# Optimization experiments

Hardware: AMD Instinct MI355X
Metric: run time of the kernel (lower is better)

Reference implementation:

```python
import jax, jax.numpy as jnp
import numpy as np

NODE_DIM = 128
N_NODES = 100000
N_EDGES = 600000


def setup_inputs() -> dict:
    key = jax.random.key(0)
    k_x, k_e, k_w1, k_b1, k_w2, k_b2 = jax.random.split(key, 6)
    x = jax.random.normal(k_x, (N_NODES, NODE_DIM), dtype=jnp.float32)
    edge_index = jax.random.randint(k_e, (2, N_EDGES), 0, N_NODES, dtype=jnp.int64)
    # nn.Linear default init: U(-1/sqrt(fan_in), 1/sqrt(fan_in))
    lim1 = 1.0 / np.sqrt(2 * NODE_DIM)
    W1 = jax.random.uniform(k_w1, (2 * NODE_DIM, NODE_DIM), minval=-lim1, maxval=lim1, dtype=jnp.float32)
    b1 = jax.random.uniform(k_b1, (NODE_DIM,), minval=-lim1, maxval=lim1, dtype=jnp.float32)
    lim2 = 1.0 / np.sqrt(NODE_DIM)
    W2 = jax.random.uniform(k_w2, (NODE_DIM, 1), minval=-lim2, maxval=lim2, dtype=jnp.float32)
    b2 = jax.random.uniform(k_b2, (1,), minval=-lim2, maxval=lim2, dtype=jnp.float32)
    return {"x": x, "edge_index": edge_index, "W1": W1, "b1": b1, "W2": W2, "b2": b2}


def reference(x, edge_index, W1, b1, W2, b2):
    src = edge_index[0]
    dst = edge_index[1]
    # [E, 2*node_dim] gathered pair features
    pair = jnp.concatenate([x[src], x[dst]], axis=-1)
    h = jax.nn.relu(pair @ W1 + b1)          # [E, node_dim]
    s = jax.nn.sigmoid(h @ W2 + b2)          # [E, 1]
    return s.squeeze(-1)                      # [E]
```

## Files before the change

### kernel.cpp

```cpp
#include <hip/hip_runtime.h>
#include <hip/hip_bf16.h>
#include <stdint.h>

#define NODE_DIM 128
#define N_NODES  100000
#define N_EDGES  600000
#define NOUT     256

typedef __bf16 bf16x8 __attribute__((ext_vector_type(8)));
typedef float  f32x4  __attribute__((ext_vector_type(4)));

static __device__ inline unsigned pack2_bf16(float a, float b) {
    unsigned short ua = __builtin_bit_cast(unsigned short, (__bf16)a);
    unsigned short ub = __builtin_bit_cast(unsigned short, (__bf16)b);
    return (unsigned)ua | ((unsigned)ub << 16);
}

static __device__ __forceinline__ void async_copy16(const float* g, void* l) {
    __builtin_amdgcn_global_load_lds(
        (__attribute__((address_space(1))) void*)(uintptr_t)g,
        (__attribute__((address_space(3))) void*)(uint32_t)(uintptr_t)l,
        16, 0, 0);
}

__global__ void wprep_kernel(const float* __restrict__ W1, __bf16* __restrict__ Wt) {
    int i = blockIdx.x * 256 + threadIdx.x;
    if (i >= NOUT * NODE_DIM) return;
    int kp = i >> 7;
    int n  = i & 127;
    float v = W1[i];
    int np = (kp < NODE_DIM) ? n  : (n + NODE_DIM);
    int k  = (kp < NODE_DIM) ? kp : (kp - NODE_DIM);
    Wt[np * NODE_DIM + k] = (__bf16)v;
}

#define MT   64
#define ELD  264

__global__ __launch_bounds__(256)
void gemm_pre_kernel(const float* __restrict__ x, const __bf16* __restrict__ Wt,
                     const float* __restrict__ b1, __bf16* __restrict__ AB) {
    __shared__ __align__(16) char lds_raw[MT * ELD * 2];
    float* Xf = (float*)lds_raw;
    __bf16 (*Ls)[ELD] = (__bf16 (*)[ELD])lds_raw;

    const int t    = threadIdx.x;
    const int wave = t >> 6;
    const int lane = t & 63;
    const int lm   = lane & 15;
    const int q    = lane >> 4;
    const int m0   = blockIdx.x * MT;
    const int n0   = wave * 64;

#pragma unroll
    for (int i = 0; i < 8; ++i) {
        const int sbase = i * 256 + wave * 64;
        const int s  = sbase + lane;
        const int R  = s >> 5;
        const int p  = s & 31;
        const int cg = p ^ (R & 7);
        int gr = m0 + R;
        if (gr > N_NODES - 1) gr = N_NODES - 1;
        async_copy16(x + (size_t)gr * NODE_DIM + cg * 4, &Xf[(size_t)sbase * 4]);
    }

    bf16x8 bfr[4][4];
#pragma unroll
    for (int nt = 0; nt < 4; ++nt) {
        const int n = n0 + nt * 16 + lm;
#pragma unroll
        for (int ks = 0; ks < 4; ++ks)
            bfr[nt][ks] = __builtin_bit_cast(bf16x8,
                *(const uint4*)(Wt + (size_t)n * NODE_DIM + ks * 32 + q * 8));
    }

    __syncthreads();

    f32x4 acc[4][4];
#pragma unroll
    for (int i = 0; i < 4; ++i)
#pragma unroll
        for (int j = 0; j < 4; ++j)
            acc[i][j] = (f32x4){0.f, 0.f, 0.f, 0.f};

#pragma unroll
    for (int mt = 0; mt < 4; ++mt) {
        const int R  = mt * 16 + lm;
        const int rs = R & 7;
#pragma unroll
        for (int ks = 0; ks < 4; ++ks) {
            const int c0 = ks * 8 + q * 2;
            const float4 f0 = *(const float4*)&Xf[(R * 32 + (c0 ^ rs)) * 4];
            const float4 f1 = *(const float4*)&Xf[(R * 32 + ((c0 + 1) ^ rs)) * 4];
            uint4 p;
            p.x = pack2_bf16(f0.x, f0.y);
            p.y = pack2_bf16(f0.z, f0.w);
            p.z = pack2_bf16(f1.x, f1.y);
            p.w = pack2_bf16(f1.z, f1.w);
            bf16x8 af = __builtin_bit_cast(bf16x8, p);
#pragma unroll
            for (int nt = 0; nt < 4; ++nt)
                acc[mt][nt] = __builtin_amdgcn_mfma_f32_16x16x32_bf16(
                    af, bfr[nt][ks], acc[mt][nt], 0, 0, 0);
        }
    }

    __syncthreads();

#pragma unroll
    for (int nt = 0; nt < 4; ++nt) {
        const int n = n0 + nt * 16 + lm;
        const float bias = (n < NODE_DIM) ? b1[n] : 0.f;
#pragma unroll
        for (int mt = 0; mt < 4; ++mt) {
#pragma unroll
            for (int r = 0; r < 4; ++r)
                Ls[mt * 16 + q * 4 + r][n] = (__bf16)(acc[mt][nt][r] + bias);
        }
    }
    __syncthreads();

    const int c8 = (t & 31) * 8;
#pragma unroll
    for (int i = 0; i < 8; ++i) {
        const int row = i * 8 + (t >> 5);
        const int m = m0 + row;
        if (m < N_NODES)
            *(uint4*)(AB + (size_t)m * NOUT + c8) = *(const uint4*)(&Ls[row][c8]);
    }
}

__global__ __launch_bounds__(256)
void edge_score_kernel(const __bf16* __restrict__ AB, const int* __restrict__ idx,
                       const float* __restrict__ W2, const float* __restrict__ b2,
                       float* __restrict__ out) {
    const int t      = threadIdx.x;
    const int sub    = t & 15;
    const int g0     = (blockIdx.x * 256 + t) >> 4;
    const int stride = (gridDim.x * 256) >> 4;

    float w[8];
#pragma unroll
    for (int j = 0; j < 8; ++j) w[j] = W2[sub * 8 + j];
    const float bias2 = b2[0];

    for (int e = g0; e < N_EDGES; e += 2 * stride) {
        const int e1   = e + stride;
        const bool h1  = e1 < N_EDGES;
        const int s0 = idx[e];
        const int d0 = idx[N_EDGES + e];
        const int s1 = h1 ? idx[e1] : s0;
        const int d1 = h1 ? idx[N_EDGES + e1] : d0;

        const uint4 av0 = *(const uint4*)(AB + (size_t)s0 * NOUT + sub * 8);
        const uint4 bv0 = *(const uint4*)(AB + (size_t)d0 * NOUT + NODE_DIM + sub * 8);
        const uint4 av1 = *(const uint4*)(AB + (size_t)s1 * NOUT + sub * 8);
        const uint4 bv1 = *(const uint4*)(AB + (size_t)d1 * NOUT + NODE_DIM + sub * 8);

        const unsigned* au0 = (const unsigned*)&av0;
        const unsigned* bu0 = (const unsigned*)&bv0;
        const unsigned* au1 = (const unsigned*)&av1;
        const unsigned* bu1 = (const unsigned*)&bv1;
        float p0 = 0.f, p1 = 0.f;
#pragma unroll
        for (int j = 0; j < 4; ++j) {
            float a0 = __builtin_bit_cast(float, au0[j] << 16);
            float a1 = __builtin_bit_cast(float, au0[j] & 0xffff0000u);
            float c0 = __builtin_bit_cast(float, bu0[j] << 16);
            float c1 = __builtin_bit_cast(float, bu0[j] & 0xffff0000u);
            p0 = fmaf(fmaxf(a0 + c0, 0.f), w[2 * j],     p0);
            p0 = fmaf(fmaxf(a1 + c1, 0.f), w[2 * j + 1], p0);
            float e0 = __builtin_bit_cast(float, au1[j] << 16);
            float e1f= __builtin_bit_cast(float, au1[j] & 0xffff0000u);
            float f0 = __builtin_bit_cast(float, bu1[j] << 16);
            float f1 = __builtin_bit_cast(float, bu1[j] & 0xffff0000u);
            p1 = fmaf(fmaxf(e0 + f0, 0.f), w[2 * j],     p1);
            p1 = fmaf(fmaxf(e1f+ f1, 0.f), w[2 * j + 1], p1);
        }
        p0 += __shfl_xor(p0, 1);  p1 += __shfl_xor(p1, 1);
        p0 += __shfl_xor(p0, 2);  p1 += __shfl_xor(p1, 2);
        p0 += __shfl_xor(p0, 4);  p1 += __shfl_xor(p1, 4);
        p0 += __shfl_xor(p0, 8);  p1 += __shfl_xor(p1, 8);
        if (sub == 0) {
            out[e] = 1.f / (1.f + __expf(-(p0 + bias2)));
            if (h1) out[e1] = 1.f / (1.f + __expf(-(p1 + bias2)));
        }
    }
}

__global__ __launch_bounds__(128)
void naive_edge_kernel(const float* __restrict__ x, const int* __restrict__ idx,
                       const float* __restrict__ W1, const float* __restrict__ b1,
                       const float* __restrict__ W2, const float* __restrict__ b2,
                       float* __restrict__ out) {
    __shared__ float pair[2 * NODE_DIM];
    __shared__ float red[2];
    int e = blockIdx.x;
    int t = threadIdx.x;
    int s = idx[e], d = idx[N_EDGES + e];
    pair[t]            = x[(size_t)s * NODE_DIM + t];
    pair[NODE_DIM + t] = x[(size_t)d * NODE_DIM + t];
    __syncthreads();
    float acc = b1[t];
    for (int k = 0; k < 2 * NODE_DIM; ++k)
        acc = fmaf(pair[k], W1[k * NODE_DIM + t], acc);
    float c = fmaxf(acc, 0.f) * W2[t];
#pragma unroll
    for (int m = 1; m < 64; m <<= 1) c += __shfl_xor(c, m);
    if ((t & 63) == 0) red[t >> 6] = c;
    __syncthreads();
    if (t == 0) out[e] = 1.f / (1.f + __expf(-(red[0] + red[1] + b2[0])));
}

extern "C" void kernel_launch(void* const* d_in, const int* in_sizes, int n_in,
                              void* d_out, int out_size, void* d_ws, size_t ws_size,
                              hipStream_t stream) {
    const float* x   = (const float*)d_in[0];
    const int*   idx = (const int*)d_in[1];
    const float* W1  = (const float*)d_in[2];
    const float* b1  = (const float*)d_in[3];
    const float* W2  = (const float*)d_in[4];
    const float* b2  = (const float*)d_in[5];
    float* out = (float*)d_out;

    const size_t ab_bytes = (size_t)N_NODES * NOUT * sizeof(__bf16);
    const size_t wt_bytes = (size_t)NOUT * NODE_DIM * sizeof(__bf16);

    if (ws_size >= ab_bytes + wt_bytes) {
        __bf16* AB = (__bf16*)d_ws;
        __bf16* Wt = (__bf16*)((char*)d_ws + ab_bytes);
        hipLaunchKernelGGL(wprep_kernel, dim3(128), dim3(256), 0, stream, W1, Wt);
        hipLaunchKernelGGL(gemm_pre_kernel, dim3((N_NODES + MT - 1) / MT), dim3(256),
                           0, stream, x, Wt, b1, AB);
        hipLaunchKernelGGL(edge_score_kernel, dim3(2048), dim3(256), 0, stream,
                           AB, idx, W2, b2, out);
    } else {
        hipLaunchKernelGGL(naive_edge_kernel, dim3(N_EDGES), dim3(128), 0, stream,
                           x, idx, W1, b1, W2, b2, out);
    }
}
```

Baseline: 154.5 us.

## Quantize per-node projection tables to int8 with per-row scales

The precompute kernel now quantizes each node's projected src and dst halves to unsigned 8-bit values with a per-row absmax scale, instead of storing bf16. The edge kernel gathers 8-byte int8 chunks plus the scalar scales and dequantizes them with FMAs. This halves the gathered bytes per edge and the table footprint, aiming to cut memory and cache traffic. It adds quantization error, which could affect accuracy tolerance, plus some extra per-element integer unpacking work.

```diff
diff --git a/kernel.cpp b/kernel.cpp
--- a/kernel.cpp
+++ b/kernel.cpp
@@ -39,7 +39,9 @@
 
 __global__ __launch_bounds__(256)
 void gemm_pre_kernel(const float* __restrict__ x, const __bf16* __restrict__ Wt,
-                     const float* __restrict__ b1, __bf16* __restrict__ AB) {
+                     const float* __restrict__ b1,
+                     unsigned char* __restrict__ Ai, unsigned char* __restrict__ Bi,
+                     float* __restrict__ sA, float* __restrict__ sB) {
     __shared__ __align__(16) char lds_raw[MT * ELD * 2];
     float* Xf = (float*)lds_raw;
     __bf16 (*Ls)[ELD] = (__bf16 (*)[ELD])lds_raw;
@@ -120,18 +122,50 @@
     }
     __syncthreads();
 
-    const int c8 = (t & 31) * 8;
-#pragma unroll
-    for (int i = 0; i < 8; ++i) {
-        const int row = i * 8 + (t >> 5);
+    const int grp = t >> 4;
+    const int sub = t & 15;
+#pragma unroll
+    for (int pass = 0; pass < 8; ++pass) {
+        const int hr   = pass * 16 + grp;
+        const int row  = hr >> 1;
+        const int half = hr & 1;
+        const uint4 v = *(const uint4*)(&Ls[row][half * 128 + sub * 8]);
+        const unsigned* vu = (const unsigned*)&v;
+        float f[8];
+#pragma unroll
+        for (int i = 0; i < 4; ++i) {
+            f[2 * i]     = __builtin_bit_cast(float, vu[i] << 16);
+            f[2 * i + 1] = __builtin_bit_cast(float, vu[i] & 0xffff0000u);
+        }
+        float am = 0.f;
+#pragma unroll
+        for (int i = 0; i < 8; ++i) am = fmaxf(am, fabsf(f[i]));
+        am = fmaxf(am, __shfl_xor(am, 1));
+        am = fmaxf(am, __shfl_xor(am, 2));
+        am = fmaxf(am, __shfl_xor(am, 4));
+        am = fmaxf(am, __shfl_xor(am, 8));
+        const float inv = (am > 0.f) ? 127.f / am : 0.f;
+        unsigned u[8];
+#pragma unroll
+        for (int i = 0; i < 8; ++i)
+            u[i] = (unsigned)(int)(f[i] * inv + 128.5f);
+        uint2 pk;
+        pk.x = u[0] | (u[1] << 8) | (u[2] << 16) | (u[3] << 24);
+        pk.y = u[4] | (u[5] << 8) | (u[6] << 16) | (u[7] << 24);
         const int m = m0 + row;
-        if (m < N_NODES)
-            *(uint4*)(AB + (size_t)m * NOUT + c8) = *(const uint4*)(&Ls[row][c8]);
+        if (m < N_NODES) {
+            unsigned char* dst = (half ? Bi : Ai) + (size_t)m * NODE_DIM + sub * 8;
+            *(uint2*)dst = pk;
+            if (sub == 0) (half ? sB : sA)[m] = am * (1.f / 127.f);
+        }
     }
 }
 
 __global__ __launch_bounds__(256)
-void edge_score_kernel(const __bf16* __restrict__ AB, const int* __restrict__ idx,
+void edge_score_kernel(const unsigned char* __restrict__ Ai,
+                       const unsigned char* __restrict__ Bi,
+                       const float* __restrict__ sA, const float* __restrict__ sB,
+                       const int* __restrict__ idx,
                        const float* __restrict__ W2, const float* __restrict__ b2,
                        float* __restrict__ out) {
     const int t      = threadIdx.x;
@@ -145,37 +179,38 @@
     const float bias2 = b2[0];
 
     for (int e = g0; e < N_EDGES; e += 2 * stride) {
-        const int e1   = e + stride;
-        const bool h1  = e1 < N_EDGES;
+        const int e1  = e + stride;
+        const bool h1 = e1 < N_EDGES;
         const int s0 = idx[e];
         const int d0 = idx[N_EDGES + e];
         const int s1 = h1 ? idx[e1] : s0;
         const int d1 = h1 ? idx[N_EDGES + e1] : d0;
 
-        const uint4 av0 = *(const uint4*)(AB + (size_t)s0 * NOUT + sub * 8);
-        const uint4 bv0 = *(const uint4*)(AB + (size_t)d0 * NOUT + NODE_DIM + sub * 8);
-        const uint4 av1 = *(const uint4*)(AB + (size_t)s1 * NOUT + sub * 8);
-        const uint4 bv1 = *(const uint4*)(AB + (size_t)d1 * NOUT + NODE_DIM + sub * 8);
-
-        const unsigned* au0 = (const unsigned*)&av0;
-        const unsigned* bu0 = (const unsigned*)&bv0;
-        const unsigned* au1 = (const unsigned*)&av1;
-        const unsigned* bu1 = (const unsigned*)&bv1;
+        const uint2 a0 = *(const uint2*)(Ai + (size_t)s0 * NODE_DIM + sub * 8);
+        const uint2 b0 = *(const uint2*)(Bi + (size_t)d0 * NODE_DIM + sub * 8);
+        const uint2 a1 = *(const uint2*)(Ai + (size_t)s1 * NODE_DIM + sub * 8);
+        const uint2 b1v= *(const uint2*)(Bi + (size_t)d1 * NODE_DIM + sub * 8);
+        const float sa0 = sA[s0], sb0 = sB[d0];
+        const float sa1 = sA[s1], sb1 = sB[d1];
+        const float c0 = -128.f * (sa0 + sb0);
+        const float c1 = -128.f * (sa1 + sb1);
+
+        const unsigned aw0[2] = {a0.x, a0.y}, bw0[2] = {b0.x, b0.y};
+        const unsigned aw1[2] = {a1.x, a1.y}, bw1[2] = {b1v.x, b1v.y};
         float p0 = 0.f, p1 = 0.f;
 #pragma unroll
-        for (int j = 0; j < 4; ++j) {
-            float a0 = __builtin_bit_cast(float, au0[j] << 16);
-            float a1 = __builtin_bit_cast(float, au0[j] & 0xffff0000u);
-            float c0 = __builtin_bit_cast(float, bu0[j] << 16);
-            float c1 = __builtin_bit_cast(float, bu0[j] & 0xffff0000u);
-            p0 = fmaf(fmaxf(a0 + c0, 0.f), w[2 * j],     p0);
-            p0 = fmaf(fmaxf(a1 + c1, 0.f), w[2 * j + 1], p0);
-            float e0 = __builtin_bit_cast(float, au1[j] << 16);
-            float e1f= __builtin_bit_cast(float, au1[j] & 0xffff0000u);
-            float f0 = __builtin_bit_cast(float, bu1[j] << 16);
-            float f1 = __builtin_bit_cast(float, bu1[j] & 0xffff0000u);
-            p1 = fmaf(fmaxf(e0 + f0, 0.f), w[2 * j],     p1);
-            p1 = fmaf(fmaxf(e1f+ f1, 0.f), w[2 * j + 1], p1);
+        for (int wd = 0; wd < 2; ++wd) {
+#pragma unroll
+            for (int k = 0; k < 4; ++k) {
+                const float ua0 = (float)((aw0[wd] >> (8 * k)) & 0xffu);
+                const float ub0 = (float)((bw0[wd] >> (8 * k)) & 0xffu);
+                const float ua1 = (float)((aw1[wd] >> (8 * k)) & 0xffu);
+                const float ub1 = (float)((bw1[wd] >> (8 * k)) & 0xffu);
+                const float h0 = fmaxf(fmaf(ua0, sa0, fmaf(ub0, sb0, c0)), 0.f);
+                const float hh = fmaxf(fmaf(ua1, sa1, fmaf(ub1, sb1, c1)), 0.f);
+                p0 = fmaf(h0, w[wd * 4 + k], p0);
+                p1 = fmaf(hh, w[wd * 4 + k], p1);
+            }
         }
         p0 += __shfl_xor(p0, 1);  p1 += __shfl_xor(p1, 1);
         p0 += __shfl_xor(p0, 2);  p1 += __shfl_xor(p1, 2);
@@ -223,17 +258,22 @@
     const float* b2  = (const float*)d_in[5];
     float* out = (float*)d_out;
 
-    const size_t ab_bytes = (size_t)N_NODES * NOUT * sizeof(__bf16);
-    const size_t wt_bytes = (size_t)NOUT * NODE_DIM * sizeof(__bf16);
-
-    if (ws_size >= ab_bytes + wt_bytes) {
-        __bf16* AB = (__bf16*)d_ws;
-        __bf16* Wt = (__bf16*)((char*)d_ws + ab_bytes);
+    const size_t tab_bytes   = (size_t)N_NODES * NODE_DIM;
+    const size_t scale_bytes = (size_t)N_NODES * sizeof(float);
+    const size_t wt_bytes    = (size_t)NOUT * NODE_DIM * sizeof(__bf16);
+    const size_t need = 2 * tab_bytes + 2 * scale_bytes + wt_bytes;
+
+    if (ws_size >= need) {
+        unsigned char* Ai = (unsigned char*)d_ws;
+        unsigned char* Bi = Ai + tab_bytes;
+        float* sA = (float*)(Bi + tab_bytes);
+        float* sB = sA + N_NODES;
+        __bf16* Wt = (__bf16*)(sB + N_NODES);
         hipLaunchKernelGGL(wprep_kernel, dim3(128), dim3(256), 0, stream, W1, Wt);
         hipLaunchKernelGGL(gemm_pre_kernel, dim3((N_NODES + MT - 1) / MT), dim3(256),
-                           0, stream, x, Wt, b1, AB);
+                           0, stream, x, Wt, b1, Ai, Bi, sA, sB);
         hipLaunchKernelGGL(edge_score_kernel, dim3(2048), dim3(256), 0, stream,
-                           AB, idx, W2, b2, out);
+                           Ai, Bi, sA, sB, idx, W2, b2, out);
     } else {
         hipLaunchKernelGGL(naive_edge_kernel, dim3(N_EDGES), dim3(128), 0, stream,
                            x, idx, W1, b1, W2, b2, out);
```

New measurement: 143.5 us. 7.1% less time.
